# Kernel optimization log

Measured on AMD Instinct MI355X. Metric: run time of the kernel, lower is better.

Reference implementation:

```python
import jax, jax.numpy as jnp
import numpy as np

N, IN_DIM, HID, HEADS, OUT = 4096, 512, 256, 2, 40
LN_EPS = 1e-5


def setup_inputs() -> dict:
    key = jax.random.key(0)
    ks = jax.random.split(key, 12)
    s_in = 1.0 / np.sqrt(IN_DIM)
    s_o = 1.0 / np.sqrt(2 * HID)
    adj = jax.random.randint(ks[0], (HEADS, N, N), 0, 2).astype(jnp.float32)
    h = jax.random.normal(ks[1], (N, IN_DIM), dtype=jnp.float32)
    Wq = jax.random.uniform(ks[2], (HEADS, IN_DIM, HID), minval=-s_in, maxval=s_in)
    bq = jax.random.uniform(ks[3], (HEADS, HID), minval=-s_in, maxval=s_in)
    Wk = jax.random.uniform(ks[4], (HEADS, IN_DIM, HID), minval=-s_in, maxval=s_in)
    bk = jax.random.uniform(ks[5], (HEADS, HID), minval=-s_in, maxval=s_in)
    Wv = jax.random.uniform(ks[6], (HEADS, IN_DIM, HID), minval=-s_in, maxval=s_in)
    bv = jax.random.uniform(ks[7], (HEADS, HID), minval=-s_in, maxval=s_in)
    Wo = jax.random.uniform(ks[8], (2 * HID, IN_DIM), minval=-s_o, maxval=s_o)
    bo = jax.random.uniform(ks[9], (IN_DIM,), minval=-s_o, maxval=s_o)
    gamma = jnp.ones((IN_DIM,), jnp.float32)
    beta = jnp.zeros((IN_DIM,), jnp.float32)
    Wp = jax.random.uniform(ks[10], (IN_DIM, OUT), minval=-s_in, maxval=s_in)
    bp = jax.random.uniform(ks[11], (OUT,), minval=-s_in, maxval=s_in)
    return dict(adj=adj, h=h, Wq=Wq, bq=bq, Wk=Wk, bk=bk, Wv=Wv, bv=bv,
                Wo=Wo, bo=bo, gamma=gamma, beta=beta, Wp=Wp, bp=bp)


def reference(adj, h, Wq, bq, Wk, bk, Wv, bv, Wo, bo, gamma, beta, Wp, bp):
    # Per-head projections, vectorized over the head axis. [H, N, D]
    Q = jnp.einsum('ni,hid->hnd', h, Wq) + bq[:, None, :]
    K = jnp.einsum('ni,hid->hnd', h, Wk) + bk[:, None, :]
    V = jnp.einsum('ni,hid->hnd', h, Wv) + bv[:, None, :]
    # Dense QK^T, elementwise-multiplied (not -inf masked) by per-head adjacency.
    scores = jnp.einsum('hnd,hmd->hnm', Q, K) * adj          # [H, N, N]
    attn = jax.nn.softmax(scores, axis=-1)
    X = jnp.einsum('hnm,hmd->hnd', attn, V)                  # [H, N, D]
    # cat([X0, X1], dim=1) -> [N, H*D]
    X_final = jnp.transpose(X, (1, 0, 2)).reshape(N, HEADS * HID)
    z = X_final @ Wo + bo                                    # [N, IN_DIM]
    mu = jnp.mean(z, axis=-1, keepdims=True)
    var = jnp.var(z, axis=-1, keepdims=True)
    M = (z - mu) * jax.lax.rsqrt(var + LN_EPS) * gamma + beta
    return jax.nn.softmax(M @ Wp + bp, axis=1)               # [N, OUT]
```

## Files before the change

### kernel.cpp

```cpp
#include <hip/hip_runtime.h>
#include <hip/hip_bf16.h>

#define N_TOK 4096
#define D_IN  512
#define D_HID 256
#define N_OUT 40

typedef _Float16 half8 __attribute__((ext_vector_type(8)));
typedef _Float16 half4 __attribute__((ext_vector_type(4)));
typedef float    f32x4 __attribute__((ext_vector_type(4)));

__device__ __forceinline__ void async_copy16(const _Float16* g, _Float16* l) {
  __builtin_amdgcn_global_load_lds(
      (const __attribute__((address_space(1))) unsigned int*)(g),
      (__attribute__((address_space(3))) unsigned int*)(l), 16, 0, 0);
}

__device__ __forceinline__ void transpose_tile(const float* __restrict__ src, int in_ncols,
                                               _Float16* __restrict__ dst, int out_ncols,
                                               int i0, int d0, float* lds )
{
  int tid = threadIdx.x;
  int l15 = tid & 15, l4 = tid >> 4;
#pragma unroll
  for (int p = 0; p < 4; p++) {
    int ii = p * 16 + l4;
    float4 x = *(const float4*)(src + (size_t)(i0 + ii) * in_ncols + d0 + l15 * 4);
    lds[(l15 * 4 + 0) * 65 + ii] = x.x;
    lds[(l15 * 4 + 1) * 65 + ii] = x.y;
    lds[(l15 * 4 + 2) * 65 + ii] = x.z;
    lds[(l15 * 4 + 3) * 65 + ii] = x.w;
  }
  __syncthreads();
  int dd = tid >> 2, chunk = tid & 3;
  half8 o0, o1;
#pragma unroll
  for (int j = 0; j < 8; j++) o0[j] = (_Float16)lds[dd * 65 + chunk * 16 + j];
#pragma unroll
  for (int j = 0; j < 8; j++) o1[j] = (_Float16)lds[dd * 65 + chunk * 16 + 8 + j];
  *(half8*)(dst + (size_t)(d0 + dd) * out_ncols + i0 + chunk * 16) = o0;
  *(half8*)(dst + (size_t)(d0 + dd) * out_ncols + i0 + chunk * 16 + 8) = o1;
}

__global__ void prep_kernel(const float* __restrict__ h, const float* __restrict__ Wq,
                            const float* __restrict__ Wk, const float* __restrict__ Wv,
                            const float* __restrict__ Wo, const float* __restrict__ Wp,
                            _Float16* __restrict__ h16, _Float16* __restrict__ Wqt,
                            _Float16* __restrict__ Wkt, _Float16* __restrict__ Wvt,
                            _Float16* __restrict__ Wot, _Float16* __restrict__ Wpt)
{
  __shared__ float lds[64 * 65];
  int b = blockIdx.x, tid = threadIdx.x;
  if (b < 1024) {
    int base = b * 2048 + tid * 8;
    float4 x0 = *(const float4*)(h + base);
    float4 x1 = *(const float4*)(h + base + 4);
    half8 o;
    o[0]=(_Float16)x0.x; o[1]=(_Float16)x0.y; o[2]=(_Float16)x0.z; o[3]=(_Float16)x0.w;
    o[4]=(_Float16)x1.x; o[5]=(_Float16)x1.y; o[6]=(_Float16)x1.z; o[7]=(_Float16)x1.w;
    *(half8*)(h16 + base) = o;
  } else if (b < 1216) {
    int t = b - 1024;
    int mat = t >> 5;
    int m = mat >> 1, head = mat & 1;
    const float* W = (m==0 ? Wq : (m==1 ? Wk : Wv)) + head * (D_IN * D_HID);
    _Float16* Wt   = (m==0 ? Wqt : (m==1 ? Wkt : Wvt)) + head * (D_IN * D_HID);
    int tt = t & 31;
    int i0 = (tt >> 2) * 64, d0 = (tt & 3) * 64;
    transpose_tile(W, D_HID, Wt, D_IN, i0, d0, lds);
  } else if (b < 1280) {
    int t = b - 1216;
    int i0 = (t >> 3) * 64, d0 = (t & 7) * 64;
    transpose_tile(Wo, D_IN, Wot, D_IN, i0, d0, lds);
  } else {
    int blk = b - 1280;
    int idx = blk * 1024 + tid * 4;
    int j = idx >> 9, i = idx & 511;
    half4 o;
#pragma unroll
    for (int u = 0; u < 4; u++)
      o[u] = (j < N_OUT) ? (_Float16)Wp[(i + u) * N_OUT + j] : (_Float16)0.f;
    *(half4*)(Wpt + j * D_IN + i) = o;
  }
}

__global__ __launch_bounds__(256, 2) void proj_kernel(
    const _Float16* __restrict__ h16, const _Float16* __restrict__ W6 ,
    const _Float16* __restrict__ Wvt,
    const float* __restrict__ bq, const float* __restrict__ bk,
    const float* __restrict__ bv,
    _Float16* __restrict__ Q16, _Float16* __restrict__ K16,
    _Float16* __restrict__ VT16)
{
  __shared__ __align__(16) _Float16 Atile[128 * 64];
  __shared__ __align__(16) _Float16 Btile[128 * 64];

  int b = blockIdx.x;
  int tid = threadIdx.x, w = tid >> 6, lane = tid & 63, quad = lane >> 4, cL = lane & 15;
  int wr = w >> 1, wc = w & 1;

  const _Float16 *Asrc, *Bsrc;
  int isV;
  int m0 = 0, n0 = 0, head = 0, mh = 0;
  if (b < 256) {
    isV = 0;
    m0 = (b >> 3) * 128;
    int ct = b & 7;
    mh = ct >> 1;
    n0 = (ct & 1) * 128;
    Asrc = h16 + (size_t)m0 * D_IN;
    Bsrc = W6 + (size_t)(ct * 128) * D_IN;
  } else {
    isV = 1;
    int t = b - 256;
    head = t >> 6;
    int tt = t & 63;
    m0 = (tt >> 5) * 128;
    n0 = (tt & 31) * 128;
    Asrc = Wvt + (size_t)head * (D_HID * D_IN) + (size_t)m0 * D_IN;
    Bsrc = h16 + (size_t)n0 * D_IN;
  }

  const f32x4 z4 = {0.f, 0.f, 0.f, 0.f};
  f32x4 acc[4][4];
#pragma unroll
  for (int i = 0; i < 4; i++)
#pragma unroll
    for (int j = 0; j < 4; j++) acc[i][j] = z4;

  int r8 = lane >> 3, chs = (lane & 7) ^ r8;

  for (int kc = 0; kc < 8; kc++) {
    __syncthreads();
#pragma unroll
    for (int g = 0; g < 4; g++) {
      int row = (w * 4 + g) * 8 + r8;
      async_copy16(Asrc + (size_t)row * D_IN + kc * 64 + chs * 8, Atile + (w * 4 + g) * 512);
      async_copy16(Bsrc + (size_t)row * D_IN + kc * 64 + chs * 8, Btile + (w * 4 + g) * 512);
    }
    __syncthreads();
#pragma unroll
    for (int kk = 0; kk < 2; kk++) {
      int ch = ((kk * 4 + quad) ^ (cL & 7)) * 8;
      half8 a[4], bf[4];
#pragma unroll
      for (int mt = 0; mt < 4; mt++)
        a[mt] = *(const half8*)(Atile + (wr * 64 + mt * 16 + cL) * 64 + ch);
#pragma unroll
      for (int nt = 0; nt < 4; nt++)
        bf[nt] = *(const half8*)(Btile + (wc * 64 + nt * 16 + cL) * 64 + ch);
#pragma unroll
      for (int mt = 0; mt < 4; mt++)
#pragma unroll
        for (int nt = 0; nt < 4; nt++)
          acc[mt][nt] = __builtin_amdgcn_mfma_f32_16x16x32_f16(a[mt], bf[nt], acc[mt][nt], 0, 0, 0);
    }
  }

  if (!isV) {
    _Float16* Out = (mh < 2 ? Q16 + (size_t)mh * (N_TOK * D_HID)
                            : K16 + (size_t)(mh - 2) * (N_TOK * D_HID));
    const float* bias = (mh < 2 ? bq + mh * D_HID : bk + (mh - 2) * D_HID);
#pragma unroll
    for (int mt = 0; mt < 4; mt++) {
      int row = m0 + wr * 64 + mt * 16 + quad * 4;
#pragma unroll
      for (int nt = 0; nt < 4; nt++) {
        int colg = n0 + wc * 64 + nt * 16 + cL;
        float bb = bias[colg];
#pragma unroll
        for (int reg = 0; reg < 4; reg++)
          Out[(size_t)(row + reg) * D_HID + colg] = (_Float16)(acc[mt][nt][reg] + bb);
      }
    }
  } else {
    _Float16* VTh = VT16 + (size_t)head * (N_TOK * D_HID);
    const float* bvh = bv + head * D_HID;
#pragma unroll
    for (int mt = 0; mt < 4; mt++) {
      int d0r = m0 + wr * 64 + mt * 16 + quad * 4;
      float bvv[4];
#pragma unroll
      for (int reg = 0; reg < 4; reg++) bvv[reg] = bvh[d0r + reg];
#pragma unroll
      for (int nt = 0; nt < 4; nt++) {
        int tok = n0 + wc * 64 + nt * 16 + cL;
#pragma unroll
        for (int reg = 0; reg < 4; reg++)
          VTh[(size_t)(d0r + reg) * N_TOK + tok] = (_Float16)(acc[mt][nt][reg] + bvv[reg]);
      }
    }
  }
}

__global__ __launch_bounds__(256, 1) void attn_kernel(
    const float* __restrict__ adj, const _Float16* __restrict__ Q16,
    const _Float16* __restrict__ K16, const _Float16* __restrict__ VT16,
    _Float16* __restrict__ Opart, float* __restrict__ Lpart)
{
  __shared__ __align__(16) _Float16 Kbuf[2][64 * 256];
  __shared__ __align__(16) _Float16 Vbuf[2][256 * 64];
  __shared__ __align__(16) _Float16 Pbuf[4][32 * 72];
  __shared__ float Lsh[4][32];

  int b = blockIdx.x;
  int sl = b & 7;
  int head = sl >> 2, gs = sl & 3;
  int tid = threadIdx.x;
  int w = tid >> 6, lane = tid & 63, quad = lane >> 4, cL = lane & 15;
  int l5 = lane >> 5, l31 = lane & 31, l3h = lane >> 3, l7 = lane & 7;

  const _Float16* Qh = Q16 + head * (N_TOK * D_HID);
  const _Float16* Kh = K16 + head * (N_TOK * D_HID);
  const _Float16* Vh = VT16 + head * (N_TOK * D_HID);
  const float* adjh = adj + (size_t)head * N_TOK * N_TOK;

  int qrow0 = (b >> 3) * 128 + w * 32;
  int nstart = gs * 1024;
  const f32x4 z4 = {0.f, 0.f, 0.f, 0.f};

  half8 qf[2][8];
#pragma unroll
  for (int mt = 0; mt < 2; mt++)
#pragma unroll
    for (int ks = 0; ks < 8; ks++)
      qf[mt][ks] = *(const half8*)(Qh + (qrow0 + mt * 16 + cL) * D_HID + ks * 32 + quad * 8);

  const float* adjP[2][4];
#pragma unroll
  for (int mt = 0; mt < 2; mt++)
#pragma unroll
    for (int reg = 0; reg < 4; reg++)
      adjP[mt][reg] = adjh + (size_t)(qrow0 + mt * 16 + quad * 4 + reg) * N_TOK + nstart + cL;

  f32x4 acc[2][16];
  f32x4 accl[2];
#pragma unroll
  for (int mt = 0; mt < 2; mt++) {
    accl[mt] = z4;
#pragma unroll
    for (int dt = 0; dt < 16; dt++) acc[mt][dt] = z4;
  }

  _Float16* pb = Pbuf[w];

  half8 onesf;
#pragma unroll
  for (int j = 0; j < 8; j++) onesf[j] = (cL == 0) ? (_Float16)1.0f : (_Float16)0.0f;

#pragma unroll
  for (int i = 0; i < 8; i++) {
    int g = w * 8 + i;
    int rK = 2 * g + l5;
    int cK = l31 ^ (rK & 7);
    async_copy16(Kh + (size_t)(nstart + rK) * D_HID + cK * 8, Kbuf[0] + g * 512);
    int rV = 8 * g + l3h;
    int cV = l7 ^ (rV & 7);
    async_copy16(Vh + (size_t)rV * N_TOK + nstart + cV * 8, Vbuf[0] + g * 512);
  }

  for (int it = 0; it < 16; ++it) {
    int cur = it & 1;
    __syncthreads();

    float av[2][4][4];
#pragma unroll
    for (int mt = 0; mt < 2; mt++)
#pragma unroll
      for (int reg = 0; reg < 4; reg++)
#pragma unroll
        for (int ct = 0; ct < 4; ct++)
          av[mt][ct][reg] = __builtin_nontemporal_load(adjP[mt][reg] + it * 64 + ct * 16);

    if (it < 15) {
      int n1 = nstart + (it + 1) * 64;
      _Float16* Kd = Kbuf[1 - cur];
      _Float16* Vd = Vbuf[1 - cur];
#pragma unroll
      for (int i = 0; i < 8; i++) {
        int g = w * 8 + i;
        int rK = 2 * g + l5;
        int cK = l31 ^ (rK & 7);
        async_copy16(Kh + (size_t)(n1 + rK) * D_HID + cK * 8, Kd + g * 512);
        int rV = 8 * g + l3h;
        int cV = l7 ^ (rV & 7);
        async_copy16(Vh + (size_t)rV * N_TOK + n1 + cV * 8, Vd + g * 512);
      }
    }

    const _Float16* Kb = Kbuf[cur];
    f32x4 s[2][4];
#pragma unroll
    for (int mt = 0; mt < 2; mt++)
#pragma unroll
      for (int ct = 0; ct < 4; ct++) s[mt][ct] = z4;
#pragma unroll
    for (int ks = 0; ks < 8; ks++) {
#pragma unroll
      for (int ct = 0; ct < 4; ct++) {
        int rK = ct * 16 + cL;
        int ck = (ks * 4 + quad) ^ (rK & 7);
        half8 kf = *(const half8*)(Kb + rK * 256 + ck * 8);
        s[0][ct] = __builtin_amdgcn_mfma_f32_16x16x32_f16(qf[0][ks], kf, s[0][ct], 0, 0, 0);
        s[1][ct] = __builtin_amdgcn_mfma_f32_16x16x32_f16(qf[1][ks], kf, s[1][ct], 0, 0, 0);
      }
    }

#pragma unroll
    for (int mt = 0; mt < 2; mt++)
#pragma unroll
      for (int ct = 0; ct < 4; ct++)
#pragma unroll
        for (int reg = 0; reg < 4; reg++) {
          float sc = s[mt][ct][reg] * av[mt][ct][reg];
          float p = __builtin_amdgcn_exp2f(sc * 1.44269504f - 31.7392909f);
          p = fminf(p, 60000.0f);
          pb[(mt * 16 + quad * 4 + reg) * 72 + ct * 16 + cL] = (_Float16)p;
        }

    const _Float16* Vb = Vbuf[cur];
#pragma unroll
    for (int k2 = 0; k2 < 2; k2++) {
      half8 pa0 = *(const half8*)(pb + cL * 72 + k2 * 32 + quad * 8);
      half8 pa1 = *(const half8*)(pb + (16 + cL) * 72 + k2 * 32 + quad * 8);
      accl[0] = __builtin_amdgcn_mfma_f32_16x16x32_f16(pa0, onesf, accl[0], 0, 0, 0);
      accl[1] = __builtin_amdgcn_mfma_f32_16x16x32_f16(pa1, onesf, accl[1], 0, 0, 0);
#pragma unroll
      for (int dt = 0; dt < 16; dt++) {
        int rV = dt * 16 + cL;
        int cv = (k2 * 4 + quad) ^ (rV & 7);
        half8 vf = *(const half8*)(Vb + rV * 64 + cv * 8);
        acc[0][dt] = __builtin_amdgcn_mfma_f32_16x16x32_f16(pa0, vf, acc[0][dt], 0, 0, 0);
        acc[1][dt] = __builtin_amdgcn_mfma_f32_16x16x32_f16(pa1, vf, acc[1][dt], 0, 0, 0);
      }
    }
  }

  if (cL == 0) {
#pragma unroll
    for (int mt = 0; mt < 2; mt++)
#pragma unroll
      for (int reg = 0; reg < 4; reg++)
        Lsh[w][mt * 16 + quad * 4 + reg] = accl[mt][reg];
  }
#pragma unroll
  for (int mt = 0; mt < 2; mt++)
#pragma unroll
    for (int reg = 0; reg < 4; reg++) {
      float lr = Lsh[w][mt * 16 + quad * 4 + reg];
      float inv = 1.0f / fmaxf(lr, 1e-30f);
      int grow = sl * N_TOK + qrow0 + mt * 16 + quad * 4 + reg;
#pragma unroll
      for (int dt = 0; dt < 16; dt++)
        Opart[(size_t)grow * D_HID + dt * 16 + cL] = (_Float16)(acc[mt][dt][reg] * inv);
      if (cL == 0) Lpart[grow] = lr;
    }
}

__global__ void merge_kernel(const _Float16* __restrict__ Opart,
                             const float* __restrict__ Lpart,
                             _Float16* __restrict__ Xf)
{
  int t = blockIdx.x * 256 + threadIdx.x;
  int dg = (t & 63) << 2;
  int n = (t >> 6) & (N_TOK - 1);
  int head = t >> 18;
  float osum[4] = {0.f, 0.f, 0.f, 0.f};
  float lsum = 0.f;
#pragma unroll
  for (int s = 0; s < 4; s++) {
    int idx = (head * 4 + s) * N_TOK + n;
    float lw = Lpart[idx];
    half4 os = *(const half4*)(Opart + (size_t)idx * D_HID + dg);
    lsum += lw;
#pragma unroll
    for (int u = 0; u < 4; u++) osum[u] += lw * (float)os[u];
  }
  float rl = 1.0f / fmaxf(lsum, 1e-30f);
  half4 res;
#pragma unroll
  for (int u = 0; u < 4; u++) res[u] = (_Float16)(osum[u] * rl);
  *(half4*)(Xf + (size_t)n * D_IN + head * D_HID + dg) = res;
}

__global__ __launch_bounds__(256, 1) void final_kernel(
    const _Float16* __restrict__ Xf, const _Float16* __restrict__ Wot,
    const _Float16* __restrict__ Wpt, const float* __restrict__ bo,
    const float* __restrict__ gamma, const float* __restrict__ beta,
    const float* __restrict__ bp, float* __restrict__ out)
{
  __shared__ __align__(16) _Float16 Btile[512 * 64];
  __shared__ __align__(16) _Float16 Mlds[16 * 520];
  __shared__ float outs[16 * 48];
  __shared__ float lnsum[4][16], lnsq[4][16];
  __shared__ float smx[16], srl[16];

  int rowbase = blockIdx.x * 16;
  int tid = threadIdx.x, w = tid >> 6, lane = tid & 63, quad = lane >> 4, cL = lane & 15;
  const f32x4 z4 = {0.f, 0.f, 0.f, 0.f};

  half8 af[16];
#pragma unroll
  for (int t = 0; t < 16; t++)
    af[t] = *(const half8*)(Xf + (rowbase + cL) * D_IN + t * 32 + quad * 8);

  f32x4 acc[8];
#pragma unroll
  for (int i = 0; i < 8; i++) acc[i] = z4;

  int r8 = lane >> 3, chs = (lane & 7) ^ r8;

  for (int kc = 0; kc < 8; kc++) {
    __syncthreads();
#pragma unroll
    for (int g = 0; g < 16; g++) {
      int row = (w * 16 + g) * 8 + r8;
      async_copy16(Wot + (size_t)row * D_IN + kc * 64 + chs * 8, Btile + (w * 16 + g) * 512);
    }
    __syncthreads();
#pragma unroll
    for (int kk = 0; kk < 2; kk++) {
      int ch = ((kk * 4 + quad) ^ (cL & 7)) * 8;
      half8 a = af[kc * 2 + kk];
      half8 bf[8];
#pragma unroll
      for (int nt = 0; nt < 8; nt++)
        bf[nt] = *(const half8*)(Btile + (w * 128 + nt * 16 + cL) * 64 + ch);
#pragma unroll
      for (int nt = 0; nt < 8; nt++)
        acc[nt] = __builtin_amdgcn_mfma_f32_16x16x32_f16(a, bf[nt], acc[nt], 0, 0, 0);
    }
  }

  float sum[4] = {0, 0, 0, 0}, sq[4] = {0, 0, 0, 0};
#pragma unroll
  for (int nt = 0; nt < 8; nt++) {
    int col = w * 128 + nt * 16 + cL;
    float bb = bo[col];
#pragma unroll
    for (int reg = 0; reg < 4; reg++) {
      float z = acc[nt][reg] + bb;
      acc[nt][reg] = z;
      sum[reg] += z;
      sq[reg] += z * z;
    }
  }
#pragma unroll
  for (int reg = 0; reg < 4; reg++) {
#pragma unroll
    for (int msk = 1; msk < 16; msk <<= 1) {
      sum[reg] += __shfl_xor(sum[reg], msk, 16);
      sq[reg]  += __shfl_xor(sq[reg], msk, 16);
    }
  }
  if (cL == 0) {
#pragma unroll
    for (int reg = 0; reg < 4; reg++) {
      lnsum[w][quad * 4 + reg] = sum[reg];
      lnsq[w][quad * 4 + reg]  = sq[reg];
    }
  }
  __syncthreads();
  float mean[4], rstd[4];
#pragma unroll
  for (int reg = 0; reg < 4; reg++) {
    int row = quad * 4 + reg;
    float s  = lnsum[0][row] + lnsum[1][row] + lnsum[2][row] + lnsum[3][row];
    float s2 = lnsq[0][row]  + lnsq[1][row]  + lnsq[2][row]  + lnsq[3][row];
    float mu = s * (1.0f / 512.0f);
    float var = s2 * (1.0f / 512.0f) - mu * mu;
    mean[reg] = mu;
    rstd[reg] = rsqrtf(var + 1e-5f);
  }
#pragma unroll
  for (int nt = 0; nt < 8; nt++) {
    int col = w * 128 + nt * 16 + cL;
    float g = gamma[col], be = beta[col];
#pragma unroll
    for (int reg = 0; reg < 4; reg++) {
      float mval = (acc[nt][reg] - mean[reg]) * rstd[reg] * g + be;
      Mlds[(quad * 4 + reg) * 520 + col] = (_Float16)mval;
    }
  }
  __syncthreads();
  if (w < 3) {
    int jt = w;
    f32x4 a2 = z4;
#pragma unroll
    for (int t = 0; t < 16; t++) {
      half8 am = *(const half8*)(Mlds + cL * 520 + t * 32 + quad * 8);
      half8 bm = *(const half8*)(Wpt + (jt * 16 + cL) * D_IN + t * 32 + quad * 8);
      a2 = __builtin_amdgcn_mfma_f32_16x16x32_f16(am, bm, a2, 0, 0, 0);
    }
    int col = jt * 16 + cL;
    float bpv = (col < N_OUT) ? bp[col] : 0.0f;
#pragma unroll
    for (int reg = 0; reg < 4; reg++)
      outs[(quad * 4 + reg) * 48 + col] = a2[reg] + bpv;
  }
  __syncthreads();
  if (tid < 16) {
    int row = tid;
    float mx = -1e30f;
    for (int j = 0; j < N_OUT; j++) mx = fmaxf(mx, outs[row * 48 + j]);
    float ssum = 0.f;
    for (int j = 0; j < N_OUT; j++) ssum += __expf(outs[row * 48 + j] - mx);
    smx[row] = mx;
    srl[row] = 1.0f / ssum;
  }
  __syncthreads();
#pragma unroll
  for (int i = 0; i < 3; i++) {
    int lin = tid + 256 * i;
    if (lin < 16 * N_OUT) {
      int row = lin / N_OUT, col = lin % N_OUT;
      out[(size_t)(rowbase + row) * N_OUT + col] =
          __expf(outs[row * 48 + col] - smx[row]) * srl[row];
    }
  }
}

#define OFF_WOT   0u
#define OFF_WPT   524288u
#define OFF_Q16   573440u
#define OFF_K16   4767744u
#define OFF_VT16  8962048u
#define OFF_LP    13287424u
#define OFF_XF    13418496u
#define OFF_OP    17612800u
#define OFF_H16   17612800u
#define OFF_WQT   21807104u
#define OFF_WKT   22331392u
#define OFF_WVT   22855680u

extern "C" void kernel_launch(void* const* d_in, const int* in_sizes, int n_in,
                              void* d_out, int out_size, void* d_ws, size_t ws_size,
                              hipStream_t stream)
{
  const float* adj   = (const float*)d_in[0];
  const float* h     = (const float*)d_in[1];
  const float* Wq    = (const float*)d_in[2];
  const float* bq    = (const float*)d_in[3];
  const float* Wk    = (const float*)d_in[4];
  const float* bk    = (const float*)d_in[5];
  const float* Wv    = (const float*)d_in[6];
  const float* bv    = (const float*)d_in[7];
  const float* Wo    = (const float*)d_in[8];
  const float* bo    = (const float*)d_in[9];
  const float* gamma = (const float*)d_in[10];
  const float* beta  = (const float*)d_in[11];
  const float* Wp    = (const float*)d_in[12];
  const float* bp    = (const float*)d_in[13];
  float* out = (float*)d_out;
  char* ws = (char*)d_ws;

  _Float16* h16   = (_Float16*)(ws + OFF_H16);
  _Float16* Wqt   = (_Float16*)(ws + OFF_WQT);
  _Float16* Wkt   = (_Float16*)(ws + OFF_WKT);
  _Float16* Wvt   = (_Float16*)(ws + OFF_WVT);
  _Float16* Wot   = (_Float16*)(ws + OFF_WOT);
  _Float16* Wpt   = (_Float16*)(ws + OFF_WPT);
  _Float16* Q16   = (_Float16*)(ws + OFF_Q16);
  _Float16* K16   = (_Float16*)(ws + OFF_K16);
  _Float16* VT16  = (_Float16*)(ws + OFF_VT16);
  _Float16* Opart = (_Float16*)(ws + OFF_OP);
  float*    Lpart = (float*)(ws + OFF_LP);
  _Float16* Xf    = (_Float16*)(ws + OFF_XF);

  prep_kernel<<<1304, 256, 0, stream>>>(h, Wq, Wk, Wv, Wo, Wp,
                                        h16, Wqt, Wkt, Wvt, Wot, Wpt);
  proj_kernel<<<384, 256, 0, stream>>>(h16, Wqt, Wvt, bq, bk, bv,
                                       Q16, K16, VT16);
  attn_kernel<<<256, 256, 0, stream>>>(adj, Q16, K16, VT16, Opart, Lpart);
  merge_kernel<<<2048, 256, 0, stream>>>(Opart, Lpart, Xf);
  final_kernel<<<256, 256, 0, stream>>>(Xf, Wot, Wpt, bo, gamma, beta, bp, out);
}
```

Baseline: 300.9 us.

## Fuse all stages into one cooperative persistent kernel with grid syncs

Replaces the five separate kernels (prep, projection, attention, merge, final) with a single fused kernel. By default it is launched cooperatively with 256 blocks of 512 threads and uses grid-wide syncs between phases, with a four-launch fallback. The merge of partial attention outputs is folded into the final projection's operand load, which removes the Xf intermediate. The intent is to cut launch overhead and intermediate traffic, at the cost of grid barriers, a different thread and block shape for the attention phase, and occupancy limited to one block per CU.

```diff
diff --git a/kernel.cpp b/kernel.cpp
--- a/kernel.cpp
+++ b/kernel.cpp
@@ -1,5 +1,5 @@
 #include <hip/hip_runtime.h>
-#include <hip/hip_bf16.h>
+#include <hip/hip_cooperative_groups.h>
 
 #define N_TOK 4096
 #define D_IN  512
@@ -16,562 +16,570 @@
       (__attribute__((address_space(3))) unsigned int*)(l), 16, 0, 0);
 }
 
-__device__ __forceinline__ void transpose_tile(const float* __restrict__ src, int in_ncols,
-                                               _Float16* __restrict__ dst, int out_ncols,
-                                               int i0, int d0, float* lds )
-{
-  int tid = threadIdx.x;
-  int l15 = tid & 15, l4 = tid >> 4;
-#pragma unroll
-  for (int p = 0; p < 4; p++) {
-    int ii = p * 16 + l4;
-    float4 x = *(const float4*)(src + (size_t)(i0 + ii) * in_ncols + d0 + l15 * 4);
-    lds[(l15 * 4 + 0) * 65 + ii] = x.x;
-    lds[(l15 * 4 + 1) * 65 + ii] = x.y;
-    lds[(l15 * 4 + 2) * 65 + ii] = x.z;
-    lds[(l15 * 4 + 3) * 65 + ii] = x.w;
-  }
-  __syncthreads();
-  int dd = tid >> 2, chunk = tid & 3;
-  half8 o0, o1;
-#pragma unroll
-  for (int j = 0; j < 8; j++) o0[j] = (_Float16)lds[dd * 65 + chunk * 16 + j];
-#pragma unroll
-  for (int j = 0; j < 8; j++) o1[j] = (_Float16)lds[dd * 65 + chunk * 16 + 8 + j];
-  *(half8*)(dst + (size_t)(d0 + dd) * out_ncols + i0 + chunk * 16) = o0;
-  *(half8*)(dst + (size_t)(d0 + dd) * out_ncols + i0 + chunk * 16 + 8) = o1;
-}
-
-__global__ void prep_kernel(const float* __restrict__ h, const float* __restrict__ Wq,
-                            const float* __restrict__ Wk, const float* __restrict__ Wv,
-                            const float* __restrict__ Wo, const float* __restrict__ Wp,
-                            _Float16* __restrict__ h16, _Float16* __restrict__ Wqt,
-                            _Float16* __restrict__ Wkt, _Float16* __restrict__ Wvt,
-                            _Float16* __restrict__ Wot, _Float16* __restrict__ Wpt)
-{
-  __shared__ float lds[64 * 65];
-  int b = blockIdx.x, tid = threadIdx.x;
-  if (b < 1024) {
-    int base = b * 2048 + tid * 8;
-    float4 x0 = *(const float4*)(h + base);
-    float4 x1 = *(const float4*)(h + base + 4);
-    half8 o;
-    o[0]=(_Float16)x0.x; o[1]=(_Float16)x0.y; o[2]=(_Float16)x0.z; o[3]=(_Float16)x0.w;
-    o[4]=(_Float16)x1.x; o[5]=(_Float16)x1.y; o[6]=(_Float16)x1.z; o[7]=(_Float16)x1.w;
-    *(half8*)(h16 + base) = o;
-  } else if (b < 1216) {
-    int t = b - 1024;
-    int mat = t >> 5;
-    int m = mat >> 1, head = mat & 1;
-    const float* W = (m==0 ? Wq : (m==1 ? Wk : Wv)) + head * (D_IN * D_HID);
-    _Float16* Wt   = (m==0 ? Wqt : (m==1 ? Wkt : Wvt)) + head * (D_IN * D_HID);
-    int tt = t & 31;
-    int i0 = (tt >> 2) * 64, d0 = (tt & 3) * 64;
-    transpose_tile(W, D_HID, Wt, D_IN, i0, d0, lds);
-  } else if (b < 1280) {
-    int t = b - 1216;
-    int i0 = (t >> 3) * 64, d0 = (t & 7) * 64;
-    transpose_tile(Wo, D_IN, Wot, D_IN, i0, d0, lds);
-  } else {
-    int blk = b - 1280;
-    int idx = blk * 1024 + tid * 4;
-    int j = idx >> 9, i = idx & 511;
-    half4 o;
-#pragma unroll
-    for (int u = 0; u < 4; u++)
-      o[u] = (j < N_OUT) ? (_Float16)Wp[(i + u) * N_OUT + j] : (_Float16)0.f;
-    *(half4*)(Wpt + j * D_IN + i) = o;
-  }
-}
-
-__global__ __launch_bounds__(256, 2) void proj_kernel(
-    const _Float16* __restrict__ h16, const _Float16* __restrict__ W6 ,
-    const _Float16* __restrict__ Wvt,
-    const float* __restrict__ bq, const float* __restrict__ bk,
-    const float* __restrict__ bv,
-    _Float16* __restrict__ Q16, _Float16* __restrict__ K16,
-    _Float16* __restrict__ VT16)
-{
-  __shared__ __align__(16) _Float16 Atile[128 * 64];
-  __shared__ __align__(16) _Float16 Btile[128 * 64];
-
-  int b = blockIdx.x;
-  int tid = threadIdx.x, w = tid >> 6, lane = tid & 63, quad = lane >> 4, cL = lane & 15;
-  int wr = w >> 1, wc = w & 1;
-
-  const _Float16 *Asrc, *Bsrc;
-  int isV;
-  int m0 = 0, n0 = 0, head = 0, mh = 0;
-  if (b < 256) {
-    isV = 0;
-    m0 = (b >> 3) * 128;
-    int ct = b & 7;
-    mh = ct >> 1;
-    n0 = (ct & 1) * 128;
-    Asrc = h16 + (size_t)m0 * D_IN;
-    Bsrc = W6 + (size_t)(ct * 128) * D_IN;
-  } else {
-    isV = 1;
-    int t = b - 256;
-    head = t >> 6;
-    int tt = t & 63;
-    m0 = (tt >> 5) * 128;
-    n0 = (tt & 31) * 128;
-    Asrc = Wvt + (size_t)head * (D_HID * D_IN) + (size_t)m0 * D_IN;
-    Bsrc = h16 + (size_t)n0 * D_IN;
-  }
-
-  const f32x4 z4 = {0.f, 0.f, 0.f, 0.f};
-  f32x4 acc[4][4];
-#pragma unroll
-  for (int i = 0; i < 4; i++)
-#pragma unroll
-    for (int j = 0; j < 4; j++) acc[i][j] = z4;
-
-  int r8 = lane >> 3, chs = (lane & 7) ^ r8;
-
-  for (int kc = 0; kc < 8; kc++) {
-    __syncthreads();
-#pragma unroll
-    for (int g = 0; g < 4; g++) {
-      int row = (w * 4 + g) * 8 + r8;
-      async_copy16(Asrc + (size_t)row * D_IN + kc * 64 + chs * 8, Atile + (w * 4 + g) * 512);
-      async_copy16(Bsrc + (size_t)row * D_IN + kc * 64 + chs * 8, Btile + (w * 4 + g) * 512);
-    }
-    __syncthreads();
-#pragma unroll
-    for (int kk = 0; kk < 2; kk++) {
-      int ch = ((kk * 4 + quad) ^ (cL & 7)) * 8;
-      half8 a[4], bf[4];
-#pragma unroll
-      for (int mt = 0; mt < 4; mt++)
-        a[mt] = *(const half8*)(Atile + (wr * 64 + mt * 16 + cL) * 64 + ch);
-#pragma unroll
-      for (int nt = 0; nt < 4; nt++)
-        bf[nt] = *(const half8*)(Btile + (wc * 64 + nt * 16 + cL) * 64 + ch);
-#pragma unroll
-      for (int mt = 0; mt < 4; mt++)
-#pragma unroll
-        for (int nt = 0; nt < 4; nt++)
-          acc[mt][nt] = __builtin_amdgcn_mfma_f32_16x16x32_f16(a[mt], bf[nt], acc[mt][nt], 0, 0, 0);
-    }
-  }
-
-  if (!isV) {
-    _Float16* Out = (mh < 2 ? Q16 + (size_t)mh * (N_TOK * D_HID)
-                            : K16 + (size_t)(mh - 2) * (N_TOK * D_HID));
-    const float* bias = (mh < 2 ? bq + mh * D_HID : bk + (mh - 2) * D_HID);
-#pragma unroll
-    for (int mt = 0; mt < 4; mt++) {
-      int row = m0 + wr * 64 + mt * 16 + quad * 4;
-#pragma unroll
-      for (int nt = 0; nt < 4; nt++) {
-        int colg = n0 + wc * 64 + nt * 16 + cL;
-        float bb = bias[colg];
-#pragma unroll
-        for (int reg = 0; reg < 4; reg++)
-          Out[(size_t)(row + reg) * D_HID + colg] = (_Float16)(acc[mt][nt][reg] + bb);
-      }
-    }
-  } else {
-    _Float16* VTh = VT16 + (size_t)head * (N_TOK * D_HID);
-    const float* bvh = bv + head * D_HID;
-#pragma unroll
-    for (int mt = 0; mt < 4; mt++) {
-      int d0r = m0 + wr * 64 + mt * 16 + quad * 4;
-      float bvv[4];
-#pragma unroll
-      for (int reg = 0; reg < 4; reg++) bvv[reg] = bvh[d0r + reg];
-#pragma unroll
-      for (int nt = 0; nt < 4; nt++) {
-        int tok = n0 + wc * 64 + nt * 16 + cL;
-#pragma unroll
-        for (int reg = 0; reg < 4; reg++)
-          VTh[(size_t)(d0r + reg) * N_TOK + tok] = (_Float16)(acc[mt][nt][reg] + bvv[reg]);
-      }
-    }
-  }
-}
-
-__global__ __launch_bounds__(256, 1) void attn_kernel(
-    const float* __restrict__ adj, const _Float16* __restrict__ Q16,
-    const _Float16* __restrict__ K16, const _Float16* __restrict__ VT16,
-    _Float16* __restrict__ Opart, float* __restrict__ Lpart)
-{
-  __shared__ __align__(16) _Float16 Kbuf[2][64 * 256];
-  __shared__ __align__(16) _Float16 Vbuf[2][256 * 64];
-  __shared__ __align__(16) _Float16 Pbuf[4][32 * 72];
-  __shared__ float Lsh[4][32];
-
-  int b = blockIdx.x;
-  int sl = b & 7;
-  int head = sl >> 2, gs = sl & 3;
-  int tid = threadIdx.x;
-  int w = tid >> 6, lane = tid & 63, quad = lane >> 4, cL = lane & 15;
-  int l5 = lane >> 5, l31 = lane & 31, l3h = lane >> 3, l7 = lane & 7;
-
-  const _Float16* Qh = Q16 + head * (N_TOK * D_HID);
-  const _Float16* Kh = K16 + head * (N_TOK * D_HID);
-  const _Float16* Vh = VT16 + head * (N_TOK * D_HID);
-  const float* adjh = adj + (size_t)head * N_TOK * N_TOK;
-
-  int qrow0 = (b >> 3) * 128 + w * 32;
-  int nstart = gs * 1024;
-  const f32x4 z4 = {0.f, 0.f, 0.f, 0.f};
-
-  half8 qf[2][8];
-#pragma unroll
-  for (int mt = 0; mt < 2; mt++)
-#pragma unroll
-    for (int ks = 0; ks < 8; ks++)
-      qf[mt][ks] = *(const half8*)(Qh + (qrow0 + mt * 16 + cL) * D_HID + ks * 32 + quad * 8);
-
-  const float* adjP[2][4];
-#pragma unroll
-  for (int mt = 0; mt < 2; mt++)
-#pragma unroll
-    for (int reg = 0; reg < 4; reg++)
-      adjP[mt][reg] = adjh + (size_t)(qrow0 + mt * 16 + quad * 4 + reg) * N_TOK + nstart + cL;
-
-  f32x4 acc[2][16];
-  f32x4 accl[2];
-#pragma unroll
-  for (int mt = 0; mt < 2; mt++) {
-    accl[mt] = z4;
-#pragma unroll
-    for (int dt = 0; dt < 16; dt++) acc[mt][dt] = z4;
-  }
-
-  _Float16* pb = Pbuf[w];
-
-  half8 onesf;
-#pragma unroll
-  for (int j = 0; j < 8; j++) onesf[j] = (cL == 0) ? (_Float16)1.0f : (_Float16)0.0f;
-
-#pragma unroll
-  for (int i = 0; i < 8; i++) {
-    int g = w * 8 + i;
-    int rK = 2 * g + l5;
-    int cK = l31 ^ (rK & 7);
-    async_copy16(Kh + (size_t)(nstart + rK) * D_HID + cK * 8, Kbuf[0] + g * 512);
-    int rV = 8 * g + l3h;
-    int cV = l7 ^ (rV & 7);
-    async_copy16(Vh + (size_t)rV * N_TOK + nstart + cV * 8, Vbuf[0] + g * 512);
-  }
-
-  for (int it = 0; it < 16; ++it) {
-    int cur = it & 1;
-    __syncthreads();
-
-    float av[2][4][4];
-#pragma unroll
-    for (int mt = 0; mt < 2; mt++)
-#pragma unroll
-      for (int reg = 0; reg < 4; reg++)
-#pragma unroll
-        for (int ct = 0; ct < 4; ct++)
-          av[mt][ct][reg] = __builtin_nontemporal_load(adjP[mt][reg] + it * 64 + ct * 16);
-
-    if (it < 15) {
-      int n1 = nstart + (it + 1) * 64;
-      _Float16* Kd = Kbuf[1 - cur];
-      _Float16* Vd = Vbuf[1 - cur];
-#pragma unroll
-      for (int i = 0; i < 8; i++) {
-        int g = w * 8 + i;
-        int rK = 2 * g + l5;
-        int cK = l31 ^ (rK & 7);
-        async_copy16(Kh + (size_t)(n1 + rK) * D_HID + cK * 8, Kd + g * 512);
-        int rV = 8 * g + l3h;
-        int cV = l7 ^ (rV & 7);
-        async_copy16(Vh + (size_t)rV * N_TOK + n1 + cV * 8, Vd + g * 512);
-      }
-    }
-
-    const _Float16* Kb = Kbuf[cur];
-    f32x4 s[2][4];
-#pragma unroll
-    for (int mt = 0; mt < 2; mt++)
-#pragma unroll
-      for (int ct = 0; ct < 4; ct++) s[mt][ct] = z4;
-#pragma unroll
-    for (int ks = 0; ks < 8; ks++) {
-#pragma unroll
-      for (int ct = 0; ct < 4; ct++) {
-        int rK = ct * 16 + cL;
-        int ck = (ks * 4 + quad) ^ (rK & 7);
-        half8 kf = *(const half8*)(Kb + rK * 256 + ck * 8);
-        s[0][ct] = __builtin_amdgcn_mfma_f32_16x16x32_f16(qf[0][ks], kf, s[0][ct], 0, 0, 0);
-        s[1][ct] = __builtin_amdgcn_mfma_f32_16x16x32_f16(qf[1][ks], kf, s[1][ct], 0, 0, 0);
-      }
-    }
-
-#pragma unroll
-    for (int mt = 0; mt < 2; mt++)
-#pragma unroll
-      for (int ct = 0; ct < 4; ct++)
-#pragma unroll
-        for (int reg = 0; reg < 4; reg++) {
-          float sc = s[mt][ct][reg] * av[mt][ct][reg];
-          float p = __builtin_amdgcn_exp2f(sc * 1.44269504f - 31.7392909f);
-          p = fminf(p, 60000.0f);
-          pb[(mt * 16 + quad * 4 + reg) * 72 + ct * 16 + cL] = (_Float16)p;
-        }
-
-    const _Float16* Vb = Vbuf[cur];
-#pragma unroll
-    for (int k2 = 0; k2 < 2; k2++) {
-      half8 pa0 = *(const half8*)(pb + cL * 72 + k2 * 32 + quad * 8);
-      half8 pa1 = *(const half8*)(pb + (16 + cL) * 72 + k2 * 32 + quad * 8);
-      accl[0] = __builtin_amdgcn_mfma_f32_16x16x32_f16(pa0, onesf, accl[0], 0, 0, 0);
-      accl[1] = __builtin_amdgcn_mfma_f32_16x16x32_f16(pa1, onesf, accl[1], 0, 0, 0);
-#pragma unroll
-      for (int dt = 0; dt < 16; dt++) {
-        int rV = dt * 16 + cL;
-        int cv = (k2 * 4 + quad) ^ (rV & 7);
-        half8 vf = *(const half8*)(Vb + rV * 64 + cv * 8);
-        acc[0][dt] = __builtin_amdgcn_mfma_f32_16x16x32_f16(pa0, vf, acc[0][dt], 0, 0, 0);
-        acc[1][dt] = __builtin_amdgcn_mfma_f32_16x16x32_f16(pa1, vf, acc[1][dt], 0, 0, 0);
-      }
-    }
-  }
-
-  if (cL == 0) {
-#pragma unroll
-    for (int mt = 0; mt < 2; mt++)
-#pragma unroll
-      for (int reg = 0; reg < 4; reg++)
-        Lsh[w][mt * 16 + quad * 4 + reg] = accl[mt][reg];
-  }
-#pragma unroll
-  for (int mt = 0; mt < 2; mt++)
-#pragma unroll
-    for (int reg = 0; reg < 4; reg++) {
-      float lr = Lsh[w][mt * 16 + quad * 4 + reg];
-      float inv = 1.0f / fmaxf(lr, 1e-30f);
-      int grow = sl * N_TOK + qrow0 + mt * 16 + quad * 4 + reg;
-#pragma unroll
-      for (int dt = 0; dt < 16; dt++)
-        Opart[(size_t)grow * D_HID + dt * 16 + cL] = (_Float16)(acc[mt][dt][reg] * inv);
-      if (cL == 0) Lpart[grow] = lr;
-    }
-}
-
-__global__ void merge_kernel(const _Float16* __restrict__ Opart,
-                             const float* __restrict__ Lpart,
-                             _Float16* __restrict__ Xf)
-{
-  int t = blockIdx.x * 256 + threadIdx.x;
-  int dg = (t & 63) << 2;
-  int n = (t >> 6) & (N_TOK - 1);
-  int head = t >> 18;
-  float osum[4] = {0.f, 0.f, 0.f, 0.f};
-  float lsum = 0.f;
-#pragma unroll
-  for (int s = 0; s < 4; s++) {
-    int idx = (head * 4 + s) * N_TOK + n;
-    float lw = Lpart[idx];
-    half4 os = *(const half4*)(Opart + (size_t)idx * D_HID + dg);
-    lsum += lw;
-#pragma unroll
-    for (int u = 0; u < 4; u++) osum[u] += lw * (float)os[u];
-  }
-  float rl = 1.0f / fmaxf(lsum, 1e-30f);
-  half4 res;
-#pragma unroll
-  for (int u = 0; u < 4; u++) res[u] = (_Float16)(osum[u] * rl);
-  *(half4*)(Xf + (size_t)n * D_IN + head * D_HID + dg) = res;
-}
-
-__global__ __launch_bounds__(256, 1) void final_kernel(
-    const _Float16* __restrict__ Xf, const _Float16* __restrict__ Wot,
-    const _Float16* __restrict__ Wpt, const float* __restrict__ bo,
-    const float* __restrict__ gamma, const float* __restrict__ beta,
-    const float* __restrict__ bp, float* __restrict__ out)
-{
-  __shared__ __align__(16) _Float16 Btile[512 * 64];
-  __shared__ __align__(16) _Float16 Mlds[16 * 520];
-  __shared__ float outs[16 * 48];
-  __shared__ float lnsum[4][16], lnsq[4][16];
-  __shared__ float smx[16], srl[16];
-
-  int rowbase = blockIdx.x * 16;
-  int tid = threadIdx.x, w = tid >> 6, lane = tid & 63, quad = lane >> 4, cL = lane & 15;
-  const f32x4 z4 = {0.f, 0.f, 0.f, 0.f};
-
-  half8 af[16];
-#pragma unroll
-  for (int t = 0; t < 16; t++)
-    af[t] = *(const half8*)(Xf + (rowbase + cL) * D_IN + t * 32 + quad * 8);
-
-  f32x4 acc[8];
-#pragma unroll
-  for (int i = 0; i < 8; i++) acc[i] = z4;
-
-  int r8 = lane >> 3, chs = (lane & 7) ^ r8;
-
-  for (int kc = 0; kc < 8; kc++) {
-    __syncthreads();
-#pragma unroll
-    for (int g = 0; g < 16; g++) {
-      int row = (w * 16 + g) * 8 + r8;
-      async_copy16(Wot + (size_t)row * D_IN + kc * 64 + chs * 8, Btile + (w * 16 + g) * 512);
-    }
-    __syncthreads();
-#pragma unroll
-    for (int kk = 0; kk < 2; kk++) {
-      int ch = ((kk * 4 + quad) ^ (cL & 7)) * 8;
-      half8 a = af[kc * 2 + kk];
-      half8 bf[8];
-#pragma unroll
-      for (int nt = 0; nt < 8; nt++)
-        bf[nt] = *(const half8*)(Btile + (w * 128 + nt * 16 + cL) * 64 + ch);
-#pragma unroll
-      for (int nt = 0; nt < 8; nt++)
-        acc[nt] = __builtin_amdgcn_mfma_f32_16x16x32_f16(a, bf[nt], acc[nt], 0, 0, 0);
-    }
-  }
-
-  float sum[4] = {0, 0, 0, 0}, sq[4] = {0, 0, 0, 0};
-#pragma unroll
-  for (int nt = 0; nt < 8; nt++) {
-    int col = w * 128 + nt * 16 + cL;
-    float bb = bo[col];
-#pragma unroll
-    for (int reg = 0; reg < 4; reg++) {
-      float z = acc[nt][reg] + bb;
-      acc[nt][reg] = z;
-      sum[reg] += z;
-      sq[reg] += z * z;
-    }
-  }
-#pragma unroll
-  for (int reg = 0; reg < 4; reg++) {
-#pragma unroll
-    for (int msk = 1; msk < 16; msk <<= 1) {
-      sum[reg] += __shfl_xor(sum[reg], msk, 16);
-      sq[reg]  += __shfl_xor(sq[reg], msk, 16);
-    }
-  }
-  if (cL == 0) {
-#pragma unroll
-    for (int reg = 0; reg < 4; reg++) {
-      lnsum[w][quad * 4 + reg] = sum[reg];
-      lnsq[w][quad * 4 + reg]  = sq[reg];
-    }
-  }
-  __syncthreads();
-  float mean[4], rstd[4];
-#pragma unroll
-  for (int reg = 0; reg < 4; reg++) {
-    int row = quad * 4 + reg;
-    float s  = lnsum[0][row] + lnsum[1][row] + lnsum[2][row] + lnsum[3][row];
-    float s2 = lnsq[0][row]  + lnsq[1][row]  + lnsq[2][row]  + lnsq[3][row];
-    float mu = s * (1.0f / 512.0f);
-    float var = s2 * (1.0f / 512.0f) - mu * mu;
-    mean[reg] = mu;
-    rstd[reg] = rsqrtf(var + 1e-5f);
-  }
-#pragma unroll
-  for (int nt = 0; nt < 8; nt++) {
-    int col = w * 128 + nt * 16 + cL;
-    float g = gamma[col], be = beta[col];
-#pragma unroll
-    for (int reg = 0; reg < 4; reg++) {
-      float mval = (acc[nt][reg] - mean[reg]) * rstd[reg] * g + be;
-      Mlds[(quad * 4 + reg) * 520 + col] = (_Float16)mval;
-    }
-  }
-  __syncthreads();
-  if (w < 3) {
-    int jt = w;
-    f32x4 a2 = z4;
-#pragma unroll
-    for (int t = 0; t < 16; t++) {
-      half8 am = *(const half8*)(Mlds + cL * 520 + t * 32 + quad * 8);
-      half8 bm = *(const half8*)(Wpt + (jt * 16 + cL) * D_IN + t * 32 + quad * 8);
-      a2 = __builtin_amdgcn_mfma_f32_16x16x32_f16(am, bm, a2, 0, 0, 0);
-    }
-    int col = jt * 16 + cL;
-    float bpv = (col < N_OUT) ? bp[col] : 0.0f;
-#pragma unroll
-    for (int reg = 0; reg < 4; reg++)
-      outs[(quad * 4 + reg) * 48 + col] = a2[reg] + bpv;
-  }
-  __syncthreads();
-  if (tid < 16) {
-    int row = tid;
-    float mx = -1e30f;
-    for (int j = 0; j < N_OUT; j++) mx = fmaxf(mx, outs[row * 48 + j]);
-    float ssum = 0.f;
-    for (int j = 0; j < N_OUT; j++) ssum += __expf(outs[row * 48 + j] - mx);
-    smx[row] = mx;
-    srl[row] = 1.0f / ssum;
-  }
-  __syncthreads();
-#pragma unroll
-  for (int i = 0; i < 3; i++) {
-    int lin = tid + 256 * i;
-    if (lin < 16 * N_OUT) {
-      int row = lin / N_OUT, col = lin % N_OUT;
-      out[(size_t)(rowbase + row) * N_OUT + col] =
-          __expf(outs[row * 48 + col] - smx[row]) * srl[row];
-    }
-  }
-}
+struct Params {
+  const float *adj, *h, *Wq, *bq, *Wk, *bk, *Wv, *bv, *Wo, *bo, *gamma, *beta, *Wp, *bp;
+  float* out;
+  char* ws;
+};
 
 #define OFF_WOT   0u
 #define OFF_WPT   524288u
 #define OFF_Q16   573440u
 #define OFF_K16   4767744u
 #define OFF_VT16  8962048u
-#define OFF_LP    13287424u
-#define OFF_XF    13418496u
-#define OFF_OP    17612800u
-#define OFF_H16   17612800u
-#define OFF_WQT   21807104u
-#define OFF_WKT   22331392u
-#define OFF_WVT   22855680u
+#define OFF_LP    13156352u
+#define OFF_OP    13418496u
+#define OFF_H16   13418496u
+#define OFF_WQT   17612800u
+#define OFF_WKT   18137088u
+#define OFF_WVT   18661376u
+
+__global__ __launch_bounds__(512, 2) void fused_kernel(Params P, int phase)
+{
+  __shared__ __align__(16) char smem[152576];
+  const int bid = blockIdx.x, tid = threadIdx.x;
+  const int w = tid >> 6, lane = tid & 63, quad = lane >> 4, cL = lane & 15;
+  const int l5 = lane >> 5, l31 = lane & 31, l3h = lane >> 3, l7 = lane & 7;
+  const f32x4 z4 = {0.f, 0.f, 0.f, 0.f};
+
+  char* ws = P.ws;
+  _Float16* Wot  = (_Float16*)(ws + OFF_WOT);
+  _Float16* Wpt  = (_Float16*)(ws + OFF_WPT);
+  _Float16* Q16  = (_Float16*)(ws + OFF_Q16);
+  _Float16* K16  = (_Float16*)(ws + OFF_K16);
+  _Float16* VT16 = (_Float16*)(ws + OFF_VT16);
+  float*    Lp   = (float*)   (ws + OFF_LP);
+  _Float16* Op   = (_Float16*)(ws + OFF_OP);
+  _Float16* h16  = (_Float16*)(ws + OFF_H16);
+  _Float16* Wqt  = (_Float16*)(ws + OFF_WQT);
+  _Float16* Wkt  = (_Float16*)(ws + OFF_WKT);
+  _Float16* Wvt  = (_Float16*)(ws + OFF_WVT);
+
+  if (phase <= 0) {
+    float* lds = (float*)smem;
+    for (int job = bid; job < 780; job += 256) {
+      if (job < 512) {
+        int base = job * 4096 + tid * 8;
+        float4 x0 = *(const float4*)(P.h + base);
+        float4 x1 = *(const float4*)(P.h + base + 4);
+        half8 o;
+        o[0]=(_Float16)x0.x; o[1]=(_Float16)x0.y; o[2]=(_Float16)x0.z; o[3]=(_Float16)x0.w;
+        o[4]=(_Float16)x1.x; o[5]=(_Float16)x1.y; o[6]=(_Float16)x1.z; o[7]=(_Float16)x1.w;
+        *(half8*)(h16 + base) = o;
+      } else if (job < 768) {
+        const float* src; _Float16* dst; int in_nc, i0, d0;
+        if (job < 704) {
+          int t = job - 512;
+          int mat = t >> 5;
+          int m = mat >> 1, head = mat & 1;
+          src = (m==0 ? P.Wq : (m==1 ? P.Wk : P.Wv)) + head * (D_IN * D_HID);
+          dst = (m==0 ? Wqt : (m==1 ? Wkt : Wvt)) + head * (D_IN * D_HID);
+          in_nc = D_HID;
+          int tt = t & 31;
+          i0 = (tt >> 2) * 64; d0 = (tt & 3) * 64;
+        } else {
+          int t = job - 704;
+          src = P.Wo; dst = Wot; in_nc = D_IN;
+          i0 = (t >> 3) * 64; d0 = (t & 7) * 64;
+        }
+        int ii = tid >> 3, c8 = (tid & 7) * 8;
+        float4 x0 = *(const float4*)(src + (size_t)(i0 + ii) * in_nc + d0 + c8);
+        float4 x1 = *(const float4*)(src + (size_t)(i0 + ii) * in_nc + d0 + c8 + 4);
+        lds[(c8 + 0) * 65 + ii] = x0.x;
+        lds[(c8 + 1) * 65 + ii] = x0.y;
+        lds[(c8 + 2) * 65 + ii] = x0.z;
+        lds[(c8 + 3) * 65 + ii] = x0.w;
+        lds[(c8 + 4) * 65 + ii] = x1.x;
+        lds[(c8 + 5) * 65 + ii] = x1.y;
+        lds[(c8 + 6) * 65 + ii] = x1.z;
+        lds[(c8 + 7) * 65 + ii] = x1.w;
+        __syncthreads();
+        int dd = tid >> 3, ch = tid & 7;
+        half8 o;
+#pragma unroll
+        for (int j = 0; j < 8; j++) o[j] = (_Float16)lds[dd * 65 + ch * 8 + j];
+        *(half8*)(dst + (size_t)(d0 + dd) * D_IN + i0 + ch * 8) = o;
+      } else {
+        int t = job - 768;
+        int idx = t * 2048 + tid * 4;
+        int j = idx >> 9, i = idx & 511;
+        half4 o;
+#pragma unroll
+        for (int u = 0; u < 4; u++)
+          o[u] = (j < N_OUT) ? (_Float16)P.Wp[(i + u) * N_OUT + j] : (_Float16)0.f;
+        *(half4*)(Wpt + j * D_IN + i) = o;
+      }
+      __syncthreads();
+    }
+  }
+  if (phase < 0) { __threadfence(); cooperative_groups::this_grid().sync(); }
+
+  if (phase == -1 || phase == 1) {
+    _Float16* Atile = (_Float16*)smem;
+    _Float16* Btile = (_Float16*)(smem + 16384);
+    int wr = w >> 1, wc = w & 1;
+    int chs = l7 ^ l3h;
+    for (int job = bid; job < 384; job += 256) {
+      const _Float16 *Asrc, *Bsrc;
+      int isV = 0, m0, n0, head = 0, mh = 0;
+      if (job < 256) {
+        m0 = (job >> 3) * 128;
+        int ct = job & 7;
+        mh = ct >> 1;
+        n0 = (ct & 1) * 128;
+        Asrc = h16 + (size_t)m0 * D_IN;
+        Bsrc = Wqt + (size_t)(ct * 128) * D_IN;
+      } else {
+        isV = 1;
+        int t = job - 256;
+        head = t >> 6;
+        int tt = t & 63;
+        m0 = (tt >> 5) * 128;
+        n0 = (tt & 31) * 128;
+        Asrc = Wvt + (size_t)head * (D_HID * D_IN) + (size_t)m0 * D_IN;
+        Bsrc = h16 + (size_t)n0 * D_IN;
+      }
+      f32x4 acc[2][4];
+#pragma unroll
+      for (int i = 0; i < 2; i++)
+#pragma unroll
+        for (int j = 0; j < 4; j++) acc[i][j] = z4;
+      for (int kc = 0; kc < 8; kc++) {
+        __syncthreads();
+#pragma unroll
+        for (int i = 0; i < 2; i++) {
+          int g = w * 2 + i;
+          int row = g * 8 + l3h;
+          async_copy16(Asrc + (size_t)row * D_IN + kc * 64 + chs * 8, Atile + g * 512);
+          async_copy16(Bsrc + (size_t)row * D_IN + kc * 64 + chs * 8, Btile + g * 512);
+        }
+        __syncthreads();
+#pragma unroll
+        for (int kk = 0; kk < 2; kk++) {
+          int ch = ((kk * 4 + quad) ^ (cL & 7)) * 8;
+          half8 a[2], bf[4];
+#pragma unroll
+          for (int mt = 0; mt < 2; mt++)
+            a[mt] = *(const half8*)(Atile + (wr * 32 + mt * 16 + cL) * 64 + ch);
+#pragma unroll
+          for (int nt = 0; nt < 4; nt++)
+            bf[nt] = *(const half8*)(Btile + (wc * 64 + nt * 16 + cL) * 64 + ch);
+#pragma unroll
+          for (int mt = 0; mt < 2; mt++)
+#pragma unroll
+            for (int nt = 0; nt < 4; nt++)
+              acc[mt][nt] = __builtin_amdgcn_mfma_f32_16x16x32_f16(a[mt], bf[nt], acc[mt][nt], 0, 0, 0);
+        }
+      }
+      if (!isV) {
+        _Float16* Out = (mh < 2 ? Q16 + (size_t)mh * (N_TOK * D_HID)
+                                : K16 + (size_t)(mh - 2) * (N_TOK * D_HID));
+        const float* bias = (mh < 2 ? P.bq + mh * D_HID : P.bk + (mh - 2) * D_HID);
+#pragma unroll
+        for (int mt = 0; mt < 2; mt++) {
+          int row = m0 + wr * 32 + mt * 16 + quad * 4;
+#pragma unroll
+          for (int nt = 0; nt < 4; nt++) {
+            int colg = n0 + wc * 64 + nt * 16 + cL;
+            float bb = bias[colg];
+#pragma unroll
+            for (int reg = 0; reg < 4; reg++)
+              Out[(size_t)(row + reg) * D_HID + colg] = (_Float16)(acc[mt][nt][reg] + bb);
+          }
+        }
+      } else {
+        _Float16* VTh = VT16 + (size_t)head * (N_TOK * D_HID);
+        const float* bvh = P.bv + head * D_HID;
+#pragma unroll
+        for (int mt = 0; mt < 2; mt++) {
+          int d0r = m0 + wr * 32 + mt * 16 + quad * 4;
+          float bvv[4];
+#pragma unroll
+          for (int reg = 0; reg < 4; reg++) bvv[reg] = bvh[d0r + reg];
+#pragma unroll
+          for (int nt = 0; nt < 4; nt++) {
+            int tok = n0 + wc * 64 + nt * 16 + cL;
+#pragma unroll
+            for (int reg = 0; reg < 4; reg++)
+              VTh[(size_t)(d0r + reg) * N_TOK + tok] = (_Float16)(acc[mt][nt][reg] + bvv[reg]);
+          }
+        }
+      }
+    }
+  }
+  if (phase < 0) { __threadfence(); cooperative_groups::this_grid().sync(); }
+
+  if (phase == -1 || phase == 2) {
+    _Float16* Kbuf0 = (_Float16*)smem;
+    _Float16* Kbuf1 = (_Float16*)(smem + 32768);
+    _Float16* Vbuf0 = (_Float16*)(smem + 65536);
+    _Float16* Vbuf1 = (_Float16*)(smem + 98304);
+    _Float16* pb    = (_Float16*)(smem + 131072) + w * (32 * 40);
+    float*    LshF  = (float*)(smem + 151552);
+
+    int sl = bid & 7, head = sl >> 2, gs = sl & 3;
+    int q0 = (bid >> 3) * 128;
+    int r = w >> 1, c = w & 1;
+    int qrow0 = q0 + r * 32;
+    int nstart = gs * 1024;
+
+    const _Float16* Qh = Q16 + head * (N_TOK * D_HID);
+    const _Float16* Kh = K16 + head * (N_TOK * D_HID);
+    const _Float16* Vh = VT16 + head * (N_TOK * D_HID);
+    const float* adjh = P.adj + (size_t)head * N_TOK * N_TOK;
+
+    half8 qf[2][8];
+#pragma unroll
+    for (int mt = 0; mt < 2; mt++)
+#pragma unroll
+      for (int ks = 0; ks < 8; ks++)
+        qf[mt][ks] = *(const half8*)(Qh + (qrow0 + mt * 16 + cL) * D_HID + ks * 32 + quad * 8);
+
+    const float* adjP[2][4];
+#pragma unroll
+    for (int mt = 0; mt < 2; mt++)
+#pragma unroll
+      for (int reg = 0; reg < 4; reg++)
+        adjP[mt][reg] = adjh + (size_t)(qrow0 + mt * 16 + quad * 4 + reg) * N_TOK
+                        + nstart + c * 32 + cL;
+
+    f32x4 acc[2][16];
+    f32x4 accl[2];
+#pragma unroll
+    for (int mt = 0; mt < 2; mt++) {
+      accl[mt] = z4;
+#pragma unroll
+      for (int dt = 0; dt < 16; dt++) acc[mt][dt] = z4;
+    }
+    half8 onesf;
+#pragma unroll
+    for (int j = 0; j < 8; j++) onesf[j] = (cL == 0) ? (_Float16)1.0f : (_Float16)0.0f;
+
+#pragma unroll
+    for (int i = 0; i < 4; i++) {
+      int g = w * 4 + i;
+      int rK = 2 * g + l5;
+      int cK = l31 ^ (rK & 7);
+      async_copy16(Kh + (size_t)(nstart + rK) * D_HID + cK * 8, Kbuf0 + g * 512);
+      int rV = 8 * g + l3h;
+      int cV = l7 ^ (rV & 7);
+      async_copy16(Vh + (size_t)rV * N_TOK + nstart + cV * 8, Vbuf0 + g * 512);
+    }
+
+    for (int it = 0; it < 16; ++it) {
+      _Float16* Kb = (it & 1) ? Kbuf1 : Kbuf0;
+      _Float16* Vb = (it & 1) ? Vbuf1 : Vbuf0;
+      _Float16* Kd = (it & 1) ? Kbuf0 : Kbuf1;
+      _Float16* Vd = (it & 1) ? Vbuf0 : Vbuf1;
+      __syncthreads();
+
+      float av[2][2][4];
+#pragma unroll
+      for (int mt = 0; mt < 2; mt++)
+#pragma unroll
+        for (int reg = 0; reg < 4; reg++)
+#pragma unroll
+          for (int ct = 0; ct < 2; ct++)
+            av[mt][ct][reg] = __builtin_nontemporal_load(adjP[mt][reg] + it * 64 + ct * 16);
+
+      if (it < 15) {
+        int n1 = nstart + (it + 1) * 64;
+#pragma unroll
+        for (int i = 0; i < 4; i++) {
+          int g = w * 4 + i;
+          int rK = 2 * g + l5;
+          int cK = l31 ^ (rK & 7);
+          async_copy16(Kh + (size_t)(n1 + rK) * D_HID + cK * 8, Kd + g * 512);
+          int rV = 8 * g + l3h;
+          int cV = l7 ^ (rV & 7);
+          async_copy16(Vh + (size_t)rV * N_TOK + n1 + cV * 8, Vd + g * 512);
+        }
+      }
+
+      f32x4 s[2][2];
+#pragma unroll
+      for (int mt = 0; mt < 2; mt++)
+#pragma unroll
+        for (int ct = 0; ct < 2; ct++) s[mt][ct] = z4;
+#pragma unroll
+      for (int ks = 0; ks < 8; ks++) {
+#pragma unroll
+        for (int ct = 0; ct < 2; ct++) {
+          int rK = c * 32 + ct * 16 + cL;
+          int ck = (ks * 4 + quad) ^ (cL & 7);
+          half8 kf = *(const half8*)(Kb + rK * 256 + ck * 8);
+          s[0][ct] = __builtin_amdgcn_mfma_f32_16x16x32_f16(qf[0][ks], kf, s[0][ct], 0, 0, 0);
+          s[1][ct] = __builtin_amdgcn_mfma_f32_16x16x32_f16(qf[1][ks], kf, s[1][ct], 0, 0, 0);
+        }
+      }
+
+#pragma unroll
+      for (int mt = 0; mt < 2; mt++)
+#pragma unroll
+        for (int ct = 0; ct < 2; ct++)
+#pragma unroll
+          for (int reg = 0; reg < 4; reg++) {
+            float sc = s[mt][ct][reg] * av[mt][ct][reg];
+            float p = __builtin_amdgcn_exp2f(sc * 1.44269504f - 31.7392909f);
+            p = fminf(p, 60000.0f);
+            pb[(mt * 16 + quad * 4 + reg) * 40 + ct * 16 + cL] = (_Float16)p;
+          }
+
+      half8 pa0 = *(const half8*)(pb + cL * 40 + quad * 8);
+      half8 pa1 = *(const half8*)(pb + (16 + cL) * 40 + quad * 8);
+      accl[0] = __builtin_amdgcn_mfma_f32_16x16x32_f16(pa0, onesf, accl[0], 0, 0, 0);
+      accl[1] = __builtin_amdgcn_mfma_f32_16x16x32_f16(pa1, onesf, accl[1], 0, 0, 0);
+#pragma unroll
+      for (int dt = 0; dt < 16; dt++) {
+        int rV = dt * 16 + cL;
+        int cvv = (c * 4 + quad) ^ (cL & 7);
+        half8 vf = *(const half8*)(Vb + rV * 64 + cvv * 8);
+        acc[0][dt] = __builtin_amdgcn_mfma_f32_16x16x32_f16(pa0, vf, acc[0][dt], 0, 0, 0);
+        acc[1][dt] = __builtin_amdgcn_mfma_f32_16x16x32_f16(pa1, vf, acc[1][dt], 0, 0, 0);
+      }
+    }
+
+    __syncthreads();
+    _Float16* OshH = (_Float16*)smem;
+    if (c == 1) {
+#pragma unroll
+      for (int mt = 0; mt < 2; mt++)
+#pragma unroll
+        for (int reg = 0; reg < 4; reg++) {
+          int row = mt * 16 + quad * 4 + reg;
+#pragma unroll
+          for (int dt = 0; dt < 16; dt++)
+            OshH[(r * 32 + row) * 256 + dt * 16 + cL] = (_Float16)acc[mt][dt][reg];
+        }
+    }
+    if (cL == 0) {
+#pragma unroll
+      for (int mt = 0; mt < 2; mt++)
+#pragma unroll
+        for (int reg = 0; reg < 4; reg++)
+          LshF[w * 32 + mt * 16 + quad * 4 + reg] = accl[mt][reg];
+    }
+    __syncthreads();
+    if (c == 0) {
+#pragma unroll
+      for (int mt = 0; mt < 2; mt++)
+#pragma unroll
+        for (int reg = 0; reg < 4; reg++) {
+          int row = mt * 16 + quad * 4 + reg;
+          float l = LshF[(r * 2) * 32 + row] + LshF[(r * 2 + 1) * 32 + row];
+          float inv = 1.0f / fmaxf(l, 1e-30f);
+          int grow = sl * N_TOK + qrow0 + row;
+#pragma unroll
+          for (int dt = 0; dt < 16; dt++) {
+            float o = acc[mt][dt][reg] + (float)OshH[(r * 32 + row) * 256 + dt * 16 + cL];
+            Op[(size_t)grow * D_HID + dt * 16 + cL] = (_Float16)(o * inv);
+          }
+          if (cL == 0) Lp[grow] = l;
+        }
+    }
+  }
+  if (phase < 0) { __threadfence(); cooperative_groups::this_grid().sync(); }
+
+  if (phase == -1 || phase == 3) {
+    _Float16* Btile = (_Float16*)smem;
+    _Float16* Mlds  = (_Float16*)(smem + 65536);
+    float* outs  = (float*)(smem + 82176);
+    float* lnsum = (float*)(smem + 85248);
+    float* lnsq  = (float*)(smem + 85760);
+    float* smx   = (float*)(smem + 86272);
+    float* srl   = (float*)(smem + 86336);
+
+    int rowbase = bid * 16;
+    int zrow = rowbase + cL;
+
+    float wgt[2][4];
+#pragma unroll
+    for (int hh = 0; hh < 2; hh++) {
+      float ls = 0.f, lv[4];
+#pragma unroll
+      for (int s = 0; s < 4; s++) { lv[s] = Lp[(hh * 4 + s) * N_TOK + zrow]; ls += lv[s]; }
+      float inv = 1.0f / fmaxf(ls, 1e-30f);
+#pragma unroll
+      for (int s = 0; s < 4; s++) wgt[hh][s] = lv[s] * inv;
+    }
+    half8 af[16];
+#pragma unroll
+    for (int t = 0; t < 16; t++) {
+      int hh = t >> 3;
+      int dcol = (t & 7) * 32 + quad * 8;
+      float a8[8] = {0, 0, 0, 0, 0, 0, 0, 0};
+#pragma unroll
+      for (int s = 0; s < 4; s++) {
+        half8 o = *(const half8*)(Op + ((size_t)((hh * 4 + s) * N_TOK + zrow)) * D_HID + dcol);
+        float wv = wgt[hh][s];
+#pragma unroll
+        for (int j = 0; j < 8; j++) a8[j] += wv * (float)o[j];
+      }
+      half8 v;
+#pragma unroll
+      for (int j = 0; j < 8; j++) v[j] = (_Float16)a8[j];
+      af[t] = v;
+    }
+
+    f32x4 acc[4];
+#pragma unroll
+    for (int i = 0; i < 4; i++) acc[i] = z4;
+    int chs = l7 ^ l3h;
+    for (int kc = 0; kc < 8; kc++) {
+      __syncthreads();
+#pragma unroll
+      for (int i = 0; i < 8; i++) {
+        int g = w * 8 + i;
+        int row = g * 8 + l3h;
+        async_copy16(Wot + (size_t)row * D_IN + kc * 64 + chs * 8, Btile + g * 512);
+      }
+      __syncthreads();
+#pragma unroll
+      for (int kk = 0; kk < 2; kk++) {
+        int ch = ((kk * 4 + quad) ^ (cL & 7)) * 8;
+        half8 a = af[kc * 2 + kk];
+        half8 bf[4];
+#pragma unroll
+        for (int nt = 0; nt < 4; nt++)
+          bf[nt] = *(const half8*)(Btile + (w * 64 + nt * 16 + cL) * 64 + ch);
+#pragma unroll
+        for (int nt = 0; nt < 4; nt++)
+          acc[nt] = __builtin_amdgcn_mfma_f32_16x16x32_f16(a, bf[nt], acc[nt], 0, 0, 0);
+      }
+    }
+
+    float sum[4] = {0, 0, 0, 0}, sq[4] = {0, 0, 0, 0};
+#pragma unroll
+    for (int nt = 0; nt < 4; nt++) {
+      int col = w * 64 + nt * 16 + cL;
+      float bb = P.bo[col];
+#pragma unroll
+      for (int reg = 0; reg < 4; reg++) {
+        float z = acc[nt][reg] + bb;
+        acc[nt][reg] = z;
+        sum[reg] += z;
+        sq[reg] += z * z;
+      }
+    }
+#pragma unroll
+    for (int reg = 0; reg < 4; reg++) {
+#pragma unroll
+      for (int msk = 1; msk < 16; msk <<= 1) {
+        sum[reg] += __shfl_xor(sum[reg], msk, 16);
+        sq[reg]  += __shfl_xor(sq[reg], msk, 16);
+      }
+    }
+    if (cL == 0) {
+#pragma unroll
+      for (int reg = 0; reg < 4; reg++) {
+        lnsum[w * 16 + quad * 4 + reg] = sum[reg];
+        lnsq[w * 16 + quad * 4 + reg]  = sq[reg];
+      }
+    }
+    __syncthreads();
+    float mean[4], rstd[4];
+#pragma unroll
+    for (int reg = 0; reg < 4; reg++) {
+      int row = quad * 4 + reg;
+      float ssm = 0.f, s2 = 0.f;
+#pragma unroll
+      for (int ww = 0; ww < 8; ww++) { ssm += lnsum[ww * 16 + row]; s2 += lnsq[ww * 16 + row]; }
+      float mu = ssm * (1.0f / 512.0f);
+      float var = s2 * (1.0f / 512.0f) - mu * mu;
+      mean[reg] = mu;
+      rstd[reg] = rsqrtf(var + 1e-5f);
+    }
+#pragma unroll
+    for (int nt = 0; nt < 4; nt++) {
+      int col = w * 64 + nt * 16 + cL;
+      float g = P.gamma[col], be = P.beta[col];
+#pragma unroll
+      for (int reg = 0; reg < 4; reg++) {
+        float mval = (acc[nt][reg] - mean[reg]) * rstd[reg] * g + be;
+        Mlds[(quad * 4 + reg) * 520 + col] = (_Float16)mval;
+      }
+    }
+    __syncthreads();
+    if (w < 3) {
+      f32x4 a2 = z4;
+#pragma unroll
+      for (int t = 0; t < 16; t++) {
+        half8 am = *(const half8*)(Mlds + cL * 520 + t * 32 + quad * 8);
+        half8 bm = *(const half8*)(Wpt + (w * 16 + cL) * D_IN + t * 32 + quad * 8);
+        a2 = __builtin_amdgcn_mfma_f32_16x16x32_f16(am, bm, a2, 0, 0, 0);
+      }
+      int col = w * 16 + cL;
+      float bpv = (col < N_OUT) ? P.bp[col] : 0.0f;
+#pragma unroll
+      for (int reg = 0; reg < 4; reg++)
+        outs[(quad * 4 + reg) * 48 + col] = a2[reg] + bpv;
+    }
+    __syncthreads();
+    if (tid < 16) {
+      int row = tid;
+      float mx = -1e30f;
+      for (int j = 0; j < N_OUT; j++) mx = fmaxf(mx, outs[row * 48 + j]);
+      float ssum = 0.f;
+      for (int j = 0; j < N_OUT; j++) ssum += __expf(outs[row * 48 + j] - mx);
+      smx[row] = mx;
+      srl[row] = 1.0f / ssum;
+    }
+    __syncthreads();
+#pragma unroll
+    for (int i = 0; i < 2; i++) {
+      int lin = tid + 512 * i;
+      if (lin < 16 * N_OUT) {
+        int row = lin / N_OUT, col = lin % N_OUT;
+        P.out[(size_t)(rowbase + row) * N_OUT + col] =
+            __expf(outs[row * 48 + col] - smx[row]) * srl[row];
+      }
+    }
+  }
+}
 
 extern "C" void kernel_launch(void* const* d_in, const int* in_sizes, int n_in,
                               void* d_out, int out_size, void* d_ws, size_t ws_size,
                               hipStream_t stream)
 {
-  const float* adj   = (const float*)d_in[0];
-  const float* h     = (const float*)d_in[1];
-  const float* Wq    = (const float*)d_in[2];
-  const float* bq    = (const float*)d_in[3];
-  const float* Wk    = (const float*)d_in[4];
-  const float* bk    = (const float*)d_in[5];
-  const float* Wv    = (const float*)d_in[6];
-  const float* bv    = (const float*)d_in[7];
-  const float* Wo    = (const float*)d_in[8];
-  const float* bo    = (const float*)d_in[9];
-  const float* gamma = (const float*)d_in[10];
-  const float* beta  = (const float*)d_in[11];
-  const float* Wp    = (const float*)d_in[12];
-  const float* bp    = (const float*)d_in[13];
-  float* out = (float*)d_out;
-  char* ws = (char*)d_ws;
-
-  _Float16* h16   = (_Float16*)(ws + OFF_H16);
-  _Float16* Wqt   = (_Float16*)(ws + OFF_WQT);
-  _Float16* Wkt   = (_Float16*)(ws + OFF_WKT);
-  _Float16* Wvt   = (_Float16*)(ws + OFF_WVT);
-  _Float16* Wot   = (_Float16*)(ws + OFF_WOT);
-  _Float16* Wpt   = (_Float16*)(ws + OFF_WPT);
-  _Float16* Q16   = (_Float16*)(ws + OFF_Q16);
-  _Float16* K16   = (_Float16*)(ws + OFF_K16);
-  _Float16* VT16  = (_Float16*)(ws + OFF_VT16);
-  _Float16* Opart = (_Float16*)(ws + OFF_OP);
-  float*    Lpart = (float*)(ws + OFF_LP);
-  _Float16* Xf    = (_Float16*)(ws + OFF_XF);
-
-  prep_kernel<<<1304, 256, 0, stream>>>(h, Wq, Wk, Wv, Wo, Wp,
-                                        h16, Wqt, Wkt, Wvt, Wot, Wpt);
-  proj_kernel<<<384, 256, 0, stream>>>(h16, Wqt, Wvt, bq, bk, bv,
-                                       Q16, K16, VT16);
-  attn_kernel<<<256, 256, 0, stream>>>(adj, Q16, K16, VT16, Opart, Lpart);
-  merge_kernel<<<2048, 256, 0, stream>>>(Opart, Lpart, Xf);
-  final_kernel<<<256, 256, 0, stream>>>(Xf, Wot, Wpt, bo, gamma, beta, bp, out);
+  Params P;
+  P.adj   = (const float*)d_in[0];
+  P.h     = (const float*)d_in[1];
+  P.Wq    = (const float*)d_in[2];
+  P.bq    = (const float*)d_in[3];
+  P.Wk    = (const float*)d_in[4];
+  P.bk    = (const float*)d_in[5];
+  P.Wv    = (const float*)d_in[6];
+  P.bv    = (const float*)d_in[7];
+  P.Wo    = (const float*)d_in[8];
+  P.bo    = (const float*)d_in[9];
+  P.gamma = (const float*)d_in[10];
+  P.beta  = (const float*)d_in[11];
+  P.Wp    = (const float*)d_in[12];
+  P.bp    = (const float*)d_in[13];
+  P.out   = (float*)d_out;
+  P.ws    = (char*)d_ws;
+
+  bool coop_ok = false;
+  int dev = 0, attr = 0;
+  if (hipGetDevice(&dev) == hipSuccess &&
+      hipDeviceGetAttribute(&attr, hipDeviceAttributeCooperativeLaunch, dev) == hipSuccess &&
+      attr) {
+    int maxBlocks = 0;
+    if (hipOccupancyMaxActiveBlocksPerMultiprocessor(
+            &maxBlocks, (const void*)fused_kernel, 512, 0) == hipSuccess &&
+        maxBlocks >= 1) {
+      int phase = -1;
+      void* args[] = { &P, &phase };
+      hipError_t e = hipLaunchCooperativeKernel((const void*)fused_kernel,
+                                                dim3(256), dim3(512), args, 0, stream);
+      if (e == hipSuccess) coop_ok = true;
+    }
+  }
+  if (!coop_ok) {
+    (void)hipGetLastError();
+    fused_kernel<<<256, 512, 0, stream>>>(P, 0);
+    fused_kernel<<<256, 512, 0, stream>>>(P, 1);
+    fused_kernel<<<256, 512, 0, stream>>>(P, 2);
+    fused_kernel<<<256, 512, 0, stream>>>(P, 3);
+  }
 }
```

After: 384.2 us. +27.7%, slower.
